# Kernel optimization log

Measured on AMD Instinct MI355X. Metric: run time of the kernel, lower is better.

Reference implementation:

```python
import jax, jax.numpy as jnp
import numpy as np

B, T, D, H, F = 4, 2048, 512, 8, 2048
WINDOW = 128
HD = D // H
EPS = 1e-5


def layer_norm(x, g, b):
    mu = jnp.mean(x, axis=-1, keepdims=True)
    var = jnp.mean(jnp.square(x - mu), axis=-1, keepdims=True)
    return (x - mu) * jax.lax.rsqrt(var + EPS) * g + b


def setup_inputs() -> dict:
    key = jax.random.key(0)
    ks = jax.random.split(key, 5)
    s = 0.02
    return {
        "x": jax.random.normal(ks[0], (B, T, D), dtype=jnp.float32),
        "in_proj_w": jax.random.normal(ks[1], (3 * D, D), dtype=jnp.float32) * s,
        "in_proj_b": jnp.zeros((3 * D,), dtype=jnp.float32),
        "out_w": jax.random.normal(ks[2], (D, D), dtype=jnp.float32) * s,
        "out_b": jnp.zeros((D,), dtype=jnp.float32),
        "ln1_g": jnp.ones((D,), dtype=jnp.float32),
        "ln1_b": jnp.zeros((D,), dtype=jnp.float32),
        "ln2_g": jnp.ones((D,), dtype=jnp.float32),
        "ln2_b": jnp.zeros((D,), dtype=jnp.float32),
        "w1": jax.random.normal(ks[3], (F, D), dtype=jnp.float32) * s,
        "b1": jnp.zeros((F,), dtype=jnp.float32),
        "w2": jax.random.normal(ks[4], (D, F), dtype=jnp.float32) * s,
        "b2": jnp.zeros((D,), dtype=jnp.float32),
    }


def reference(x, in_proj_w, in_proj_b, out_w, out_b, ln1_g, ln1_b, ln2_g, ln2_b, w1, b1, w2, b2):
    # pre-norm sliding-window causal self-attention
    x2 = layer_norm(x, ln1_g, ln1_b)
    qkv = x2 @ in_proj_w.T + in_proj_b  # (B,T,3D)
    q, k, v = jnp.split(qkv, 3, axis=-1)
    q = q.reshape(B, T, H, HD)
    k = k.reshape(B, T, H, HD)
    v = v.reshape(B, T, H, HD)
    scale = 1.0 / np.sqrt(HD).astype(np.float32)
    scores = jnp.einsum("bthd,bshd->bhts", q, k) * scale  # dense (B,H,T,T)
    idx = jnp.arange(T)
    i = idx[:, None]
    j = idx[None, :]
    allowed = (j <= i) & (j >= i - WINDOW + 1)  # (T,T) bool, True = attend
    scores = jnp.where(allowed[None, None], scores, -jnp.inf)
    attn = jax.nn.softmax(scores, axis=-1)
    ctx = jnp.einsum("bhts,bshd->bthd", attn, v).reshape(B, T, D)
    attn_out = ctx @ out_w.T + out_b
    x = x + attn_out  # dropout is identity in eval
    # FFN block
    x3 = layer_norm(x, ln2_g, ln2_b)
    h = jax.nn.gelu(x3 @ w1.T + b1, approximate=False)
    x = x + h @ w2.T + b2
    return x
```

## Files before the change

kernel.cpp:

```cpp
#include <hip/hip_runtime.h>
#include <math.h>

constexpr int Bn = 4;
constexpr int Tn = 2048;
constexpr int Dn = 512;
constexpr int Hn = 8;
constexpr int HDn = 64;
constexpr int Fn = 2048;
constexpr int WIN = 128;
constexpr float EPS = 1e-5f;
constexpr int Mrows = Bn * Tn;
constexpr int QKVD = 3 * Dn;

using short8 = __attribute__((ext_vector_type(8))) short;
using f32x4  = __attribute__((ext_vector_type(4))) float;

__device__ __forceinline__ short f2bf(float f) {
    unsigned u = __float_as_uint(f);
    unsigned r = (u + 0x7FFFu + ((u >> 16) & 1u)) >> 16;
    return (short)r;
}

__device__ __forceinline__ float gelu_exact(float v) {
    return 0.5f * v * (1.0f + erff(v * 0.70710678118654752f));
}

__device__ __forceinline__ void async16(const short* g, short* l) {
    __builtin_amdgcn_global_load_lds(
        (const __attribute__((address_space(1))) void*)g,
        (__attribute__((address_space(3))) void*)l,
        16, 0, 0);
}

__global__ __launch_bounds__(256) void cvt_bf16(const float* __restrict__ src,
                                                short* __restrict__ dst, int n4)
{
    int i = blockIdx.x * 256 + threadIdx.x;
    if (i < n4) {
        float4 v = ((const float4*)src)[i];
        short4 o;
        o.x = f2bf(v.x); o.y = f2bf(v.y); o.z = f2bf(v.z); o.w = f2bf(v.w);
        ((short4*)dst)[i] = o;
    }
}

__global__ __launch_bounds__(64) void ln_kernel(const float* __restrict__ x,
                                                const float* __restrict__ g,
                                                const float* __restrict__ b,
                                                short* __restrict__ y)
{
    int row = blockIdx.x;
    int lane = threadIdx.x;
    const float4* xr = (const float4*)(x + (size_t)row * Dn);
    float4 v0 = xr[lane];
    float4 v1 = xr[lane + 64];
    float s = v0.x + v0.y + v0.z + v0.w + v1.x + v1.y + v1.z + v1.w;
#pragma unroll
    for (int off = 32; off >= 1; off >>= 1) s += __shfl_xor(s, off, 64);
    float mu = s * (1.0f / Dn);
    float d0x = v0.x - mu, d0y = v0.y - mu, d0z = v0.z - mu, d0w = v0.w - mu;
    float d1x = v1.x - mu, d1y = v1.y - mu, d1z = v1.z - mu, d1w = v1.w - mu;
    float q = d0x*d0x + d0y*d0y + d0z*d0z + d0w*d0w
            + d1x*d1x + d1y*d1y + d1z*d1z + d1w*d1w;
#pragma unroll
    for (int off = 32; off >= 1; off >>= 1) q += __shfl_xor(q, off, 64);
    float inv = rsqrtf(q * (1.0f / Dn) + EPS);
    const float4* gr = (const float4*)g;
    const float4* br = (const float4*)b;
    float4 g0 = gr[lane], g1 = gr[lane + 64];
    float4 b0 = br[lane], b1 = br[lane + 64];
    short4 a0, a1;
    a0.x = f2bf(d0x * inv * g0.x + b0.x);
    a0.y = f2bf(d0y * inv * g0.y + b0.y);
    a0.z = f2bf(d0z * inv * g0.z + b0.z);
    a0.w = f2bf(d0w * inv * g0.w + b0.w);
    a1.x = f2bf(d1x * inv * g1.x + b1.x);
    a1.y = f2bf(d1y * inv * g1.y + b1.y);
    a1.z = f2bf(d1z * inv * g1.z + b1.z);
    a1.w = f2bf(d1w * inv * g1.w + b1.w);
    short4* yr = (short4*)(y + (size_t)row * Dn);
    yr[lane] = a0;
    yr[lane + 64] = a1;
}

template <int MODE>
__global__ __launch_bounds__(256) void gemm_mfma(const short* __restrict__ A,
                                                 const short* __restrict__ Bw,
                                                 const float* __restrict__ bias,
                                                 const float* __restrict__ resid,
                                                 void* __restrict__ Cout,
                                                 short* __restrict__ q_out,
                                                 short* __restrict__ k_out,
                                                 short* __restrict__ v_out,
                                                 int M, int N, int K)
{
    __shared__ short As[2][128 * 32];
    __shared__ short Bs[2][128 * 32];
    int tid = threadIdx.x;
    int w = tid >> 6, lane = tid & 63;
    int wr = w >> 1, wc = w & 1;
    int m0 = blockIdx.y * 128, n0 = blockIdx.x * 128;
    int quad = lane >> 4, l16 = lane & 15;

    f32x4 zero = {0.f, 0.f, 0.f, 0.f};
    f32x4 acc[4][4];
#pragma unroll
    for (int i = 0; i < 4; ++i)
#pragma unroll
        for (int j = 0; j < 4; ++j) acc[i][j] = zero;

    int c0 = 2 * w;
    int rowA = lane >> 2;
    int c4 = lane & 3;
    int kcolS = (c4 ^ (rowA & 3)) * 8;
    const short* AgA = A + (size_t)(m0 + c0 * 16 + rowA) * K + kcolS;
    const short* AgB = A + (size_t)(m0 + c0 * 16 + 16 + rowA) * K + kcolS;
    const short* BgA = Bw + (size_t)(n0 + c0 * 16 + rowA) * K + kcolS;
    const short* BgB = Bw + (size_t)(n0 + c0 * 16 + 16 + rowA) * K + kcolS;

    auto stage = [&](int kt, int pp) {
        async16(AgA + kt, As[pp] + c0 * 512);
        async16(AgB + kt, As[pp] + c0 * 512 + 512);
        async16(BgA + kt, Bs[pp] + c0 * 512);
        async16(BgB + kt, Bs[pp] + c0 * 512 + 512);
    };

    stage(0, 0);
    int p = 0;
    for (int kt = 0; kt < K; kt += 32) {
        __syncthreads();
        if (kt + 32 < K) stage(kt + 32, p ^ 1);
        short8 aF[4], bF[4];
#pragma unroll
        for (int i = 0; i < 4; ++i) {
            int ra = wr * 64 + i * 16 + l16;
            int rb = wc * 64 + i * 16 + l16;
            aF[i] = *(const short8*)(As[p] + ra * 32 + ((quad ^ (l16 & 3)) * 8));
            bF[i] = *(const short8*)(Bs[p] + rb * 32 + ((quad ^ (l16 & 3)) * 8));
        }
#pragma unroll
        for (int i = 0; i < 4; ++i)
#pragma unroll
            for (int j = 0; j < 4; ++j)
                acc[i][j] = __builtin_amdgcn_mfma_f32_16x16x32_bf16(
                    aF[i], bF[j], acc[i][j], 0, 0, 0);
        p ^= 1;
    }

    if constexpr (MODE == 3) {
        __shared__ short Rep[4][64 * 68];
        short* rp = Rep[w];
        int b = m0 >> 11;
        int ncol0 = n0 + wc * 64;
        int sec = ncol0 >> 9;
        int h = (ncol0 & 511) >> 6;
        int bh = b * 8 + h;
        int t0 = (m0 & 2047) + wr * 64;
        if (sec == 2) {
#pragma unroll
            for (int j = 0; j < 4; ++j) {
                int d = j * 16 + l16;
                float bv = bias[ncol0 + j * 16 + l16];
#pragma unroll
                for (int i = 0; i < 4; ++i)
#pragma unroll
                    for (int r = 0; r < 4; ++r)
                        rp[d * 68 + i * 16 + quad * 4 + r] = f2bf(acc[i][j][r] + bv);
            }
#pragma unroll
            for (int it = 0; it < 8; ++it) {
                int row = it * 8 + (lane >> 3);
                int off = (lane & 7) * 8;
                *(short8*)(v_out + ((size_t)bh * 64 + row) * 2048 + t0 + off) =
                    *(const short8*)(rp + row * 68 + off);
            }
        } else {
            short* dst = (sec == 0 ? q_out : k_out);
#pragma unroll
            for (int j = 0; j < 4; ++j) {
                int d = j * 16 + l16;
                float bv = bias[ncol0 + j * 16 + l16];
#pragma unroll
                for (int i = 0; i < 4; ++i)
#pragma unroll
                    for (int r = 0; r < 4; ++r)
                        rp[(i * 16 + quad * 4 + r) * 68 + d] = f2bf(acc[i][j][r] + bv);
            }
#pragma unroll
            for (int it = 0; it < 8; ++it) {
                int row = it * 8 + (lane >> 3);
                int off = (lane & 7) * 8;
                *(short8*)(dst + ((size_t)bh * 2048 + t0 + row) * 64 + off) =
                    *(const short8*)(rp + row * 68 + off);
            }
        }
        return;
    }

    float* Cf = (float*)Cout;
    short* Cb = (short*)Cout;
#pragma unroll
    for (int j = 0; j < 4; ++j) {
        int n = n0 + wc * 64 + j * 16 + l16;
        float bv = bias[n];
#pragma unroll
        for (int i = 0; i < 4; ++i) {
            int mbase = m0 + wr * 64 + i * 16 + quad * 4;
#pragma unroll
            for (int r = 0; r < 4; ++r) {
                size_t idx = (size_t)(mbase + r) * N + n;
                float v = acc[i][j][r] + bv;
                if (MODE == 1) v += resid[idx];
                if (MODE == 2) {
                    Cb[idx] = f2bf(gelu_exact(v));
                } else {
                    Cf[idx] = v;
                }
            }
        }
    }
}

constexpr int QS = 72;
constexpr int VS = 200;

__global__ __launch_bounds__(256) void attn_mfma(const short* __restrict__ Qg,
                                                 const short* __restrict__ Kg,
                                                 const short* __restrict__ Vtg,
                                                 short* __restrict__ ctx)
{
    __shared__ short Qs[64 * QS];
    __shared__ short Ks[192 * QS];
    __shared__ short Vt[64 * VS];
    int tid = threadIdx.x;
    int w = tid >> 6, lane = tid & 63, quad = lane >> 4, l16 = lane & 15;
    int blk = blockIdx.x;
    int q0 = (blk & 31) << 6;
    int bh = blk >> 5;
    int kbase = q0 - 128;

    {
        const short* src = Qg + ((size_t)bh * 2048 + q0) * 64;
        for (int c = tid; c < 512; c += 256) {
            int row = c >> 3, off = (c & 7) * 8;
            *(short8*)(Qs + row * QS + off) = *(const short8*)(src + row * 64 + off);
        }
    }
    {
        const short* base = Kg + (size_t)bh * 2048 * 64;
        for (int c = tid; c < 1536; c += 256) {
            int row = c >> 3, off = (c & 7) * 8;
            int srow = kbase + row; srow = srow < 0 ? 0 : srow;
            *(short8*)(Ks + row * QS + off) = *(const short8*)(base + (size_t)srow * 64 + off);
        }
    }
    {
        const short* base = Vtg + (size_t)bh * 64 * 2048;
        for (int c = tid; c < 1536; c += 256) {
            int row = c / 24, cc = c - row * 24;
            int off = cc * 8;
            int scol = kbase + off; scol = scol < 0 ? 0 : scol;
            *(short8*)(Vt + row * VS + off) = *(const short8*)(base + (size_t)row * 2048 + scol);
        }
    }
    __syncthreads();

    short8 aF0 = *(const short8*)(Qs + (w * 16 + l16) * QS + quad * 8);
    short8 aF1 = *(const short8*)(Qs + (w * 16 + l16) * QS + 32 + quad * 8);
    f32x4 S[12];
    f32x4 zero = {0.f, 0.f, 0.f, 0.f};
#pragma unroll
    for (int t = 0; t < 12; ++t) S[t] = zero;
#pragma unroll
    for (int t = 0; t < 12; ++t) {
        short8 b0 = *(const short8*)(Ks + (t * 16 + l16) * QS + quad * 8);
        short8 b1 = *(const short8*)(Ks + (t * 16 + l16) * QS + 32 + quad * 8);
        S[t] = __builtin_amdgcn_mfma_f32_16x16x32_bf16(aF0, b0, S[t], 0, 0, 0);
        S[t] = __builtin_amdgcn_mfma_f32_16x16x32_bf16(aF1, b1, S[t], 0, 0, 0);
    }

    int i0 = w * 16 + quad * 4;
    float mrow[4] = {-INFINITY, -INFINITY, -INFINITY, -INFINITY};
#pragma unroll
    for (int t = 0; t < 12; ++t) {
        int jl = t * 16 + l16;
        int kg = kbase + jl;
#pragma unroll
        for (int r = 0; r < 4; ++r) {
            int dj = jl - (i0 + r);
            bool ok = (dj >= 1) && (dj <= 128) && (kg >= 0);
            float s = ok ? S[t][r] * 0.125f : -INFINITY;
            S[t][r] = s;
            mrow[r] = fmaxf(mrow[r], s);
        }
    }
#pragma unroll
    for (int off = 8; off >= 1; off >>= 1)
#pragma unroll
        for (int r = 0; r < 4; ++r)
            mrow[r] = fmaxf(mrow[r], __shfl_xor(mrow[r], off, 64));
    float sum[4] = {0.f, 0.f, 0.f, 0.f};
#pragma unroll
    for (int t = 0; t < 12; ++t)
#pragma unroll
        for (int r = 0; r < 4; ++r) {
            float p = __expf(S[t][r] - mrow[r]);
            S[t][r] = p;
            sum[r] += p;
        }
#pragma unroll
    for (int off = 8; off >= 1; off >>= 1)
#pragma unroll
        for (int r = 0; r < 4; ++r)
            sum[r] += __shfl_xor(sum[r], off, 64);
    float inv[4];
#pragma unroll
    for (int r = 0; r < 4; ++r) inv[r] = 1.0f / sum[r];

    __syncthreads();
    short* Ps = Ks;
#pragma unroll
    for (int t = 0; t < 12; ++t)
#pragma unroll
        for (int r = 0; r < 4; ++r)
            Ps[(w * 16 + quad * 4 + r) * VS + t * 16 + l16] = f2bf(S[t][r]);

    f32x4 O[4];
#pragma unroll
    for (int tN = 0; tN < 4; ++tN) O[tN] = zero;
#pragma unroll
    for (int s = 0; s < 6; ++s) {
        short8 aP = *(const short8*)(Ps + (w * 16 + l16) * VS + s * 32 + quad * 8);
#pragma unroll
        for (int tN = 0; tN < 4; ++tN) {
            short8 bV = *(const short8*)(Vt + (tN * 16 + l16) * VS + s * 32 + quad * 8);
            O[tN] = __builtin_amdgcn_mfma_f32_16x16x32_bf16(aP, bV, O[tN], 0, 0, 0);
        }
    }

    int b = bh >> 3, h = bh & 7;
#pragma unroll
    for (int tN = 0; tN < 4; ++tN)
#pragma unroll
        for (int r = 0; r < 4; ++r) {
            int trow = q0 + w * 16 + quad * 4 + r;
            ctx[((size_t)(b * 2048 + trow)) * 512 + h * 64 + tN * 16 + l16] =
                f2bf(O[tN][r] * inv[r]);
        }
}

extern "C" void kernel_launch(void* const* d_in, const int* in_sizes, int n_in,
                              void* d_out, int out_size, void* d_ws, size_t ws_size,
                              hipStream_t stream)
{
    const float* x         = (const float*)d_in[0];
    const float* in_proj_w = (const float*)d_in[1];
    const float* in_proj_b = (const float*)d_in[2];
    const float* out_w     = (const float*)d_in[3];
    const float* out_b     = (const float*)d_in[4];
    const float* ln1_g     = (const float*)d_in[5];
    const float* ln1_b     = (const float*)d_in[6];
    const float* ln2_g     = (const float*)d_in[7];
    const float* ln2_b     = (const float*)d_in[8];
    const float* w1        = (const float*)d_in[9];
    const float* b1        = (const float*)d_in[10];
    const float* w2        = (const float*)d_in[11];
    const float* b2        = (const float*)d_in[12];
    float* out = (float*)d_out;

    char* ws = (char*)d_ws;
    short* attnQ = (short*)ws;
    short* attnK = (short*)(ws + (size_t)8 * 1024 * 1024);
    short* attnV = (short*)(ws + (size_t)16 * 1024 * 1024);
    short* hbuf  = (short*)ws;
    short* regB  = (short*)(ws + (size_t)32 * 1024 * 1024);
    short* wq  = (short*)(ws + (size_t)40 * 1024 * 1024);
    short* wo  = wq + (size_t)QKVD * Dn;
    short* w1b = wo + (size_t)Dn * Dn;
    short* w2b = w1b + (size_t)Fn * Dn;

    cvt_bf16<<<(QKVD * Dn / 4 + 255) / 256, 256, 0, stream>>>(in_proj_w, wq, QKVD * Dn / 4);
    cvt_bf16<<<(Dn * Dn / 4 + 255) / 256, 256, 0, stream>>>(out_w, wo, Dn * Dn / 4);
    cvt_bf16<<<(Fn * Dn / 4 + 255) / 256, 256, 0, stream>>>(w1, w1b, Fn * Dn / 4);
    cvt_bf16<<<(Dn * Fn / 4 + 255) / 256, 256, 0, stream>>>(w2, w2b, Dn * Fn / 4);

    ln_kernel<<<Mrows, 64, 0, stream>>>(x, ln1_g, ln1_b, regB);
    gemm_mfma<3><<<dim3(QKVD / 128, Mrows / 128), 256, 0, stream>>>(
        regB, wq, in_proj_b, nullptr, nullptr, attnQ, attnK, attnV, Mrows, QKVD, Dn);
    attn_mfma<<<Bn * Hn * (Tn / 64), 256, 0, stream>>>(attnQ, attnK, attnV, regB);
    gemm_mfma<1><<<dim3(Dn / 128, Mrows / 128), 256, 0, stream>>>(
        regB, wo, out_b, x, out, nullptr, nullptr, nullptr, Mrows, Dn, Dn);
    ln_kernel<<<Mrows, 64, 0, stream>>>(out, ln2_g, ln2_b, regB);
    gemm_mfma<2><<<dim3(Fn / 128, Mrows / 128), 256, 0, stream>>>(
        regB, w1b, b1, nullptr, hbuf, nullptr, nullptr, nullptr, Mrows, Fn, Dn);
    gemm_mfma<1><<<dim3(Dn / 128, Mrows / 128), 256, 0, stream>>>(
        hbuf, w2b, b2, out, out, nullptr, nullptr, nullptr, Mrows, Dn, Fn);
}
```

Baseline: 260.3 us.

## Template GEMM on K-tile depth and stage GELU output through LDS

The GEMM is templated on the K tile depth, with generalized swizzled async staging and multiple MFMA k-steps per barrier. The two residual-add GEMMs (out-proj and FFN down, K=512 and K=2048) now use BK=64 to halve the number of synchronizations and raise loads in flight. Shared memory is unified into a single buffer reused for epilogues. The GELU GEMM epilogue now transposes its output through LDS so bf16 results are written as coalesced 16-byte stores instead of scattered 2-byte stores. The larger LDS footprint may reduce occupancy.

```diff
diff --git a/kernel.cpp b/kernel.cpp
--- a/kernel.cpp
+++ b/kernel.cpp
@@ -83,7 +83,7 @@
     yr[lane + 64] = a1;
 }
 
-template <int MODE>
+template <int MODE, int BK>
 __global__ __launch_bounds__(256) void gemm_mfma(const short* __restrict__ A,
                                                  const short* __restrict__ Bw,
                                                  const float* __restrict__ bias,
@@ -94,8 +94,17 @@
                                                  short* __restrict__ v_out,
                                                  int M, int N, int K)
 {
-    __shared__ short As[2][128 * 32];
-    __shared__ short Bs[2][128 * 32];
+    constexpr int NCH = BK / 8;
+    constexpr int LGN = (BK == 32) ? 2 : 3;
+    constexpr int RPI = 512 / BK;
+    constexpr int NI  = 32 / RPI;
+    constexpr int BUF = 128 * BK;
+    constexpr int KK  = BK / 32;
+    constexpr int SMSZ = (4 * BUF > 17408) ? 4 * BUF : 17408;
+    __shared__ short SMEM[SMSZ];
+    short* Asb = SMEM;
+    short* Bsb = SMEM + 2 * BUF;
+
     int tid = threadIdx.x;
     int w = tid >> 6, lane = tid & 63;
     int wr = w >> 1, wc = w & 1;
@@ -109,47 +118,58 @@
 #pragma unroll
         for (int j = 0; j < 4; ++j) acc[i][j] = zero;
 
-    int c0 = 2 * w;
-    int rowA = lane >> 2;
-    int c4 = lane & 3;
-    int kcolS = (c4 ^ (rowA & 3)) * 8;
-    const short* AgA = A + (size_t)(m0 + c0 * 16 + rowA) * K + kcolS;
-    const short* AgB = A + (size_t)(m0 + c0 * 16 + 16 + rowA) * K + kcolS;
-    const short* BgA = Bw + (size_t)(n0 + c0 * 16 + rowA) * K + kcolS;
-    const short* BgB = Bw + (size_t)(n0 + c0 * 16 + 16 + rowA) * K + kcolS;
+    int rl = lane >> LGN;
+    int ch = lane & (NCH - 1);
+    const short* Ag[NI];
+    const short* Bg[NI];
+    int ldsOff[NI];
+#pragma unroll
+    for (int s = 0; s < NI; ++s) {
+        int rowl = w * 32 + s * RPI + rl;
+        int csw = (ch ^ ((rowl * BK >> 6) & (NCH - 1))) * 8;
+        Ag[s] = A + (size_t)(m0 + rowl) * K + csw;
+        Bg[s] = Bw + (size_t)(n0 + rowl) * K + csw;
+        ldsOff[s] = (w * 32 + s * RPI) * BK;
+    }
 
     auto stage = [&](int kt, int pp) {
-        async16(AgA + kt, As[pp] + c0 * 512);
-        async16(AgB + kt, As[pp] + c0 * 512 + 512);
-        async16(BgA + kt, Bs[pp] + c0 * 512);
-        async16(BgB + kt, Bs[pp] + c0 * 512 + 512);
+#pragma unroll
+        for (int s = 0; s < NI; ++s) {
+            async16(Ag[s] + kt, Asb + pp * BUF + ldsOff[s]);
+            async16(Bg[s] + kt, Bsb + pp * BUF + ldsOff[s]);
+        }
     };
 
     stage(0, 0);
     int p = 0;
-    for (int kt = 0; kt < K; kt += 32) {
+    for (int kt = 0; kt < K; kt += BK) {
         __syncthreads();
-        if (kt + 32 < K) stage(kt + 32, p ^ 1);
-        short8 aF[4], bF[4];
-#pragma unroll
-        for (int i = 0; i < 4; ++i) {
-            int ra = wr * 64 + i * 16 + l16;
-            int rb = wc * 64 + i * 16 + l16;
-            aF[i] = *(const short8*)(As[p] + ra * 32 + ((quad ^ (l16 & 3)) * 8));
-            bF[i] = *(const short8*)(Bs[p] + rb * 32 + ((quad ^ (l16 & 3)) * 8));
-        }
-#pragma unroll
-        for (int i = 0; i < 4; ++i)
-#pragma unroll
-            for (int j = 0; j < 4; ++j)
-                acc[i][j] = __builtin_amdgcn_mfma_f32_16x16x32_bf16(
-                    aF[i], bF[j], acc[i][j], 0, 0, 0);
+        if (kt + BK < K) stage(kt + BK, p ^ 1);
+        short8 aF[KK][4], bF[KK][4];
+#pragma unroll
+        for (int kk = 0; kk < KK; ++kk)
+#pragma unroll
+            for (int i = 0; i < 4; ++i) {
+                int ra = wr * 64 + i * 16 + l16;
+                int rb = wc * 64 + i * 16 + l16;
+                int cs = ((kk * 4 + quad) ^ ((ra * BK >> 6) & (NCH - 1))) * 8;
+                aF[kk][i] = *(const short8*)(Asb + p * BUF + ra * BK + cs);
+                bF[kk][i] = *(const short8*)(Bsb + p * BUF + rb * BK + cs);
+            }
+#pragma unroll
+        for (int kk = 0; kk < KK; ++kk)
+#pragma unroll
+            for (int i = 0; i < 4; ++i)
+#pragma unroll
+                for (int j = 0; j < 4; ++j)
+                    acc[i][j] = __builtin_amdgcn_mfma_f32_16x16x32_bf16(
+                        aF[kk][i], bF[kk][j], acc[i][j], 0, 0, 0);
         p ^= 1;
     }
 
     if constexpr (MODE == 3) {
-        __shared__ short Rep[4][64 * 68];
-        short* rp = Rep[w];
+        __syncthreads();
+        short* rp = SMEM + w * 4352;
         int b = m0 >> 11;
         int ncol0 = n0 + wc * 64;
         int sec = ncol0 >> 9;
@@ -197,8 +217,31 @@
         return;
     }
 
+    if constexpr (MODE == 2) {
+        __syncthreads();
+        short* rp = SMEM + w * 4352;
+        short* Cb = (short*)Cout;
+#pragma unroll
+        for (int j = 0; j < 4; ++j) {
+            float bv = bias[n0 + wc * 64 + j * 16 + l16];
+#pragma unroll
+            for (int i = 0; i < 4; ++i)
+#pragma unroll
+                for (int r = 0; r < 4; ++r)
+                    rp[(i * 16 + quad * 4 + r) * 68 + j * 16 + l16] =
+                        f2bf(gelu_exact(acc[i][j][r] + bv));
+        }
+#pragma unroll
+        for (int it = 0; it < 8; ++it) {
+            int row = it * 8 + (lane >> 3);
+            int off = (lane & 7) * 8;
+            *(short8*)(Cb + (size_t)(m0 + wr * 64 + row) * N + n0 + wc * 64 + off) =
+                *(const short8*)(rp + row * 68 + off);
+        }
+        return;
+    }
+
     float* Cf = (float*)Cout;
-    short* Cb = (short*)Cout;
 #pragma unroll
     for (int j = 0; j < 4; ++j) {
         int n = n0 + wc * 64 + j * 16 + l16;
@@ -209,13 +252,7 @@
 #pragma unroll
             for (int r = 0; r < 4; ++r) {
                 size_t idx = (size_t)(mbase + r) * N + n;
-                float v = acc[i][j][r] + bv;
-                if (MODE == 1) v += resid[idx];
-                if (MODE == 2) {
-                    Cb[idx] = f2bf(gelu_exact(v));
-                } else {
-                    Cf[idx] = v;
-                }
+                Cf[idx] = acc[i][j][r] + bv + resid[idx];
             }
         }
     }
@@ -385,14 +422,14 @@
     cvt_bf16<<<(Dn * Fn / 4 + 255) / 256, 256, 0, stream>>>(w2, w2b, Dn * Fn / 4);
 
     ln_kernel<<<Mrows, 64, 0, stream>>>(x, ln1_g, ln1_b, regB);
-    gemm_mfma<3><<<dim3(QKVD / 128, Mrows / 128), 256, 0, stream>>>(
+    gemm_mfma<3, 32><<<dim3(QKVD / 128, Mrows / 128), 256, 0, stream>>>(
         regB, wq, in_proj_b, nullptr, nullptr, attnQ, attnK, attnV, Mrows, QKVD, Dn);
     attn_mfma<<<Bn * Hn * (Tn / 64), 256, 0, stream>>>(attnQ, attnK, attnV, regB);
-    gemm_mfma<1><<<dim3(Dn / 128, Mrows / 128), 256, 0, stream>>>(
+    gemm_mfma<1, 64><<<dim3(Dn / 128, Mrows / 128), 256, 0, stream>>>(
         regB, wo, out_b, x, out, nullptr, nullptr, nullptr, Mrows, Dn, Dn);
     ln_kernel<<<Mrows, 64, 0, stream>>>(out, ln2_g, ln2_b, regB);
-    gemm_mfma<2><<<dim3(Fn / 128, Mrows / 128), 256, 0, stream>>>(
+    gemm_mfma<2, 32><<<dim3(Fn / 128, Mrows / 128), 256, 0, stream>>>(
         regB, w1b, b1, nullptr, hbuf, nullptr, nullptr, nullptr, Mrows, Fn, Dn);
-    gemm_mfma<1><<<dim3(Dn / 128, Mrows / 128), 256, 0, stream>>>(
+    gemm_mfma<1, 64><<<dim3(Dn / 128, Mrows / 128), 256, 0, stream>>>(
         hbuf, w2b, b2, out, out, nullptr, nullptr, nullptr, Mrows, Dn, Fn);
 }
```

Measured after the change: 234.5 us. 9.9% less time.
